# Performance work log

Measured on AMD Instinct MI355X. Metric: run time of the kernel, lower is better.

Reference implementation:

```python
import jax, jax.numpy as jnp
import numpy as np

CLAMP = 2.0
SPLIT1 = 48  # split_len1 (channels - channels//2)


def _down(x):
    # pixel-unshuffle: equivalent to the grouped stride-2 conv with 0/1 kernels
    B, C, H, W = x.shape
    x = x.reshape(B, C, H // 2, 2, W // 2, 2)
    x = x.transpose(0, 1, 3, 5, 2, 4)  # (B, C, di, dj, H/2, W/2)
    return x.reshape(B, C * 4, H // 2, W // 2)


def _conv(x, w, b, stride):
    y = jax.lax.conv_general_dilated(
        x, w, window_strides=(stride, stride), padding=[(1, 1), (1, 1)],
        dimension_numbers=('NCHW', 'OIHW', 'NCHW'))
    return y + b[None, :, None, None]


def _affine(x, a):
    # forward affine coupling: x * exp(clamp*tanh(0.2*a_s)) + a_t
    ch = x.shape[1]
    sub_jac = CLAMP * jnp.tanh(0.2 * a[:, :ch])
    return x * jnp.exp(sub_jac) + a[:, ch:]


def setup_inputs() -> dict:
    key = jax.random.key(0)
    ks = jax.random.split(key, 4)
    B, C, H, W = 32, 96, 64, 64
    s1, s2 = SPLIT1, C - SPLIT1
    x = jax.random.normal(ks[0], (B, C, H, W), jnp.float32)
    # s_hi: strided 3x3 conv, split_len1 -> 8*split_len2
    w_hi = jax.random.normal(ks[1], (8 * s2, s1, 3, 3), jnp.float32) * 0.05
    b_hi = jnp.zeros((8 * s2,), jnp.float32)
    # s_lo: same-res 3x3 conv, 4*split_len2 -> 8*split_len1
    w_lo = jax.random.normal(ks[2], (8 * s1, 4 * s2, 3, 3), jnp.float32) * 0.05
    b_lo = jnp.zeros((8 * s1,), jnp.float32)
    # actnorm params: act_norm init = 10.0 * 1.0 (SOFTPLUS branch)
    ch4 = 4 * C
    act_norm = jnp.full((1, ch4, 1, 1), 10.0, jnp.float32)
    act_offset = jnp.zeros((1, ch4, 1, 1), jnp.float32)
    # hard permutation matrix (permute_soft=False), fixed seed
    rng = np.random.default_rng(0)
    perm = rng.permutation(ch4)
    pw = np.zeros((ch4, ch4), np.float32)
    pw[np.arange(ch4), perm] = 1.0
    perm_w = jnp.asarray(pw)
    return dict(x=x, w_hi=w_hi, b_hi=b_hi, w_lo=w_lo, b_lo=b_lo,
                act_norm=act_norm, act_offset=act_offset, perm_w=perm_w)


def reference(x, w_hi, b_hi, w_lo, b_lo, act_norm, act_offset, perm_w):
    x1, x2 = x[:, :SPLIT1], x[:, SPLIT1:]
    y2 = _down(x2)                     # (B, 4*s2, H/2, W/2)
    a1 = _conv(x1, w_hi, b_hi, 2)      # (B, 8*s2, H/2, W/2)
    y2 = _affine(y2, a1)
    y1 = _down(x1)                     # (B, 4*s1, H/2, W/2)
    a2 = _conv(y2, w_lo, b_lo, 1)      # (B, 8*s1, H/2, W/2)
    y1 = _affine(y1, a2)
    out = jnp.concatenate([y1, y2], axis=1)  # (B, 4*C, H/2, W/2)
    # actnorm (SOFTPLUS: 0.1 * softplus_{beta=0.5}) + hard 1x1 permutation
    scale = 0.2 * jax.nn.softplus(0.5 * act_norm)
    out = jnp.einsum('bchw,oc->bohw', out * scale + act_offset, perm_w)
    return out
```

## Files before the change

kernel.cpp:

```cpp
#include <hip/hip_runtime.h>
#include <hip/hip_bf16.h>

typedef __attribute__((ext_vector_type(8))) short s16x8;
typedef __attribute__((ext_vector_type(4))) short s16x4;
typedef __attribute__((ext_vector_type(4))) float f32x4;
typedef unsigned short u16;

#define WS_FWD    0
#define WS_INV    2048
#define WS_SCALE  4096
#define WS_OFFS   6144
#define WS_WHI    8192
#define WS_WLO    14680064
#define WS_Y2     16777216

static __device__ __forceinline__ u16 f2bf(float f) {
    __hip_bfloat16 h = __float2bfloat16(f);
    return *reinterpret_cast<u16*>(&h);
}
static __device__ __forceinline__ float bf2f(u16 u) {
    __hip_bfloat16 h = *reinterpret_cast<__hip_bfloat16*>(&u);
    return __bfloat162float(h);
}

static __device__ __forceinline__ void gl_lds16(const void* g, void* l) {
    __builtin_amdgcn_global_load_lds(
        (const __attribute__((address_space(1))) unsigned int*)g,
        (__attribute__((address_space(3))) unsigned int*)l, 16, 0, 0);
}


__global__ __launch_bounds__(256)
void k_setup(const float* __restrict__ pw, const float* __restrict__ an,
             const float* __restrict__ ao, const float* __restrict__ w_hi,
             const float* __restrict__ w_lo, int* __restrict__ fwd,
             int* __restrict__ inv, float* __restrict__ scale,
             float* __restrict__ offs, u16* __restrict__ whi,
             u16* __restrict__ wlo)
{
    const int blk = blockIdx.x;
    const int tid = threadIdx.x;
    if (blk < 288) {
        int gid = blk * 256 + tid;
        int n = gid / 192;
        int c = gid - n * 192;
        int kc = c >> 5, c32 = c & 31;
        const float* src = w_lo + (size_t)gid * 9;
#pragma unroll
        for (int t = 0; t < 9; ++t)
            wlo[((size_t)(t * 6 + kc) * 384 + n) * 32 + c32] = f2bf(src[t]);
    } else if (blk < 576) {
        int gid = (blk - 288) * 256 + tid;
        int n = gid / 192;
        int c = gid - n * 192;
        int kc = c >> 5, c32 = c & 31;
        int cin = c >> 2, dy = (c >> 1) & 1, dx = c & 1;
        const float* src = w_hi + ((size_t)n * 48 + cin) * 9;
#pragma unroll
        for (int t = 0; t < 4; ++t) {
            int th = t >> 1, tw = t & 1;
            float wv = 0.f;
            if (!(th == 0 && dy == 0) && !(tw == 0 && dx == 0)) {
                int ky = (th == 0) ? 0 : 1 + dy;
                int kx = (tw == 0) ? 0 : 1 + dx;
                wv = src[ky * 3 + kx];
            }
            whi[((size_t)(t * 6 + kc) * 384 + n) * 32 + c32] = f2bf(wv);
        }
    } else {
        int gid = (blk - 576) * 256 + tid;
        int o = gid / 384;
        int c = gid - o * 384;
        if (pw[gid] > 0.5f) { fwd[o] = c; inv[c] = o; }
        if (gid < 384) {
            scale[gid] = 0.2f * log1pf(expf(0.5f * an[gid]));
            offs[gid]  = ao[gid];
        }
    }
}

template <int T>
__global__ __launch_bounds__(256)
void f_gemm(const u16* __restrict__ in_t, const u16* __restrict__ wpk,
            const float* __restrict__ bias, const float* __restrict__ x,
            const int* __restrict__ inv, const float* __restrict__ scale,
            const float* __restrict__ offs, u16* __restrict__ y2out,
            float* __restrict__ out)
{
    const int tid = threadIdx.x;
    const int lane = tid & 63;
    const int wave = tid >> 6;
    const int l16 = lane & 15;
    const int quad = lane >> 4;
    const int mblk = blockIdx.x;
    const int b = mblk >> 4;
    const int h0 = (mblk & 15) << 1;
    const int n0 = wave * 96;

    __shared__ u16 sm[384 * 68];

    const s16x8 zero8 = {0, 0, 0, 0, 0, 0, 0, 0};

    if (T == 4) {
        for (int r = 0; r < 4; ++r) {
            int ih = h0 - 1 + r;
            if (ih >= 0 && ih < 32) {
#pragma unroll
                for (int it = 0; it < 6; ++it) {
                    int k = it * 256 + tid;
                    int cin = k >> 5;
                    int dy = (k >> 4) & 1;
                    int q = k & 15;
                    f32x4 v = *(const f32x4*)&x[((size_t)(b * 96 + cin) * 64
                                                 + (2 * ih + dy)) * 64 + q * 4];
                    int ce = cin * 4 + dy * 2;
                    int g = ce >> 3;
                    int w0 = 2 * q, w1 = w0 + 1;
                    unsigned p0 = (unsigned)f2bf(v[0]) | ((unsigned)f2bf(v[1]) << 16);
                    unsigned p1 = (unsigned)f2bf(v[2]) | ((unsigned)f2bf(v[3]) << 16);
                    *(unsigned*)&sm[r * 6144 + w0 * 192 + ((g ^ (w0 & 7)) << 3) + (ce & 7)] = p0;
                    *(unsigned*)&sm[r * 6144 + w1 * 192 + ((g ^ (w1 & 7)) << 3) + (ce & 7)] = p1;
                }
            } else {
#pragma unroll
                for (int z = 0; z < 12; ++z)
                    ((unsigned*)&sm[r * 6144])[z * 256 + tid] = 0u;
            }
        }
    } else {
        for (int r = 0; r < 4; ++r) {
            int ih = h0 - 1 + r;
            if (ih >= 0 && ih < 32) {
                const char* gsrc = (const char*)in_t + ((size_t)b * 32 + ih) * 12288;
#pragma unroll
                for (int j = 0; j < 3; ++j) {
                    int off = j * 4096 + tid * 16;
                    gl_lds16(gsrc + off, (char*)sm + r * 12288 + off);
                }
            } else {
#pragma unroll
                for (int j = 0; j < 3; ++j)
                    *(s16x8*)((char*)sm + r * 12288 + j * 4096 + tid * 16) = zero8;
            }
        }
    }
    __syncthreads();

    const f32x4 zero4 = {0.f, 0.f, 0.f, 0.f};
    f32x4 acc[4][6];
#pragma unroll
    for (int a = 0; a < 4; ++a)
#pragma unroll
        for (int c = 0; c < 6; ++c) acc[a][c] = zero4;

    for (int t = 0; t < T; ++t) {
        const int dh = (T == 4) ? ((t >> 1) - 1) : (t / 3 - 1);
        const int dw = (T == 4) ? ((t & 1) - 1) : (t % 3 - 1);
#pragma unroll
        for (int kc = 0; kc < 6; ++kc) {
            const u16* wp = wpk + ((size_t)(t * 6 + kc) * 384) * 32;
            s16x8 bf[6];
#pragma unroll
            for (int ns = 0; ns < 6; ++ns)
                bf[ns] = *(const s16x8*)(wp + (n0 + ns * 16 + l16) * 32 + quad * 8);
            const int g = kc * 4 + quad;
            s16x8 af[4];
#pragma unroll
            for (int ms = 0; ms < 4; ++ms) {
                int m = ms * 16 + l16;
                int r = (m >> 5) + dh + 1;
                int iw = (m & 31) + dw;
                int iwc = iw < 0 ? 0 : (iw > 31 ? 31 : iw);
                s16x8 v = *(const s16x8*)&sm[r * 6144 + iwc * 192 + ((g ^ (iwc & 7)) << 3)];
                if (iw != iwc) v = zero8;
                af[ms] = v;
            }
#pragma unroll
            for (int ms = 0; ms < 4; ++ms)
#pragma unroll
                for (int ns = 0; ns < 6; ++ns)
                    acc[ms][ns] = __builtin_amdgcn_mfma_f32_16x16x32_bf16(
                        af[ms], bf[ns], acc[ms][ns], 0, 0, 0);
        }
    }

    __syncthreads();

#pragma unroll
    for (int ms = 0; ms < 4; ++ms) {
#pragma unroll
        for (int ns = 0; ns < 6; ++ns) {
            int n = n0 + ns * 16 + l16;
            float bv = bias[n];
            s16x4 pk;
#pragma unroll
            for (int r4 = 0; r4 < 4; ++r4)
                pk[r4] = (short)f2bf(acc[ms][ns][r4] + bv);
            *(s16x4*)&sm[n * 68 + ms * 16 + quad * 4] = pk;
        }
    }
    __syncthreads();

    {
        const int m = lane;
        const int h = h0 + (m >> 5);
        const int w = m & 31;
        for (int i = 0; i < 48; ++i) {
            int c = wave * 48 + i;
            float a_s = bf2f(sm[c * 68 + m]);
            float a_o = bf2f(sm[(c + 192) * 68 + m]);
            int cin = (T == 4 ? 48 : 0) + (c >> 2);
            float xv = x[(((size_t)b * 96 + cin) * 64 + (2 * h + ((c >> 1) & 1))) * 64
                         + (2 * w + (c & 1))];
            float e = expf(0.4f * a_s);
            float sj = 2.f - 4.f / (e + 1.f);
            float y = xv * expf(sj) + a_o;
            int cg = (T == 4) ? (192 + c) : c;
            int o = inv[cg];
            if (T == 4) {
                u16 yb = f2bf(y);
                sm[c * 68 + m] = yb;
                out[(((size_t)b * 384 + o) * 32 + h) * 32 + w] =
                    bf2f(yb) * scale[cg] + offs[cg];
            } else {
                out[(((size_t)b * 384 + o) * 32 + h) * 32 + w] =
                    y * scale[cg] + offs[cg];
            }
        }
    }

    if (T == 4) {
        __syncthreads();
        for (int it = 0; it < 6; ++it) {
            int v = it * 256 + tid;
            int m2 = v / 24;
            int c8 = v - m2 * 24;
            int c0 = c8 * 8;
            int h2 = h0 + (m2 >> 5);
            int w2 = m2 & 31;
            s16x8 yv;
#pragma unroll
            for (int j = 0; j < 8; ++j)
                yv[j] = (short)sm[(c0 + j) * 68 + m2];
            size_t off = ((size_t)b * 32 + h2) * 6144 + w2 * 192 + ((c8 ^ (w2 & 7)) << 3);
            *(s16x8*)&y2out[off] = yv;
        }
    }
}

extern "C" void kernel_launch(void* const* d_in, const int* in_sizes, int n_in,
                              void* d_out, int out_size, void* d_ws, size_t ws_size,
                              hipStream_t stream)
{
    const float* x        = (const float*)d_in[0];
    const float* w_hi     = (const float*)d_in[1];
    const float* b_hi     = (const float*)d_in[2];
    const float* w_lo     = (const float*)d_in[3];
    const float* b_lo     = (const float*)d_in[4];
    const float* act_norm = (const float*)d_in[5];
    const float* act_off  = (const float*)d_in[6];
    const float* perm_w   = (const float*)d_in[7];
    float* out = (float*)d_out;
    char* ws = (char*)d_ws;

    int*   fwd   = (int*)(ws + WS_FWD);
    int*   inv   = (int*)(ws + WS_INV);
    float* scale = (float*)(ws + WS_SCALE);
    float* offs  = (float*)(ws + WS_OFFS);
    u16*   whi   = (u16*)(ws + WS_WHI);
    u16*   wlo   = (u16*)(ws + WS_WLO);
    u16*   y2    = (u16*)(ws + WS_Y2);

    k_setup<<<1152, 256, 0, stream>>>(perm_w, act_norm, act_off, w_hi, w_lo,
                                      fwd, inv, scale, offs, whi, wlo);
    f_gemm<4><<<512, 256, 0, stream>>>(y2, whi, b_hi, x, inv, scale, offs, y2, out);
    f_gemm<9><<<512, 256, 0, stream>>>(y2, wlo, b_lo, x, inv, scale, offs, y2, out);
}
```

Baseline: 206.4 us.

## Pack weight conversion in pairs, swizzle block order, raise MFMA priority

The setup kernel now has each thread convert two adjacent input channels and write them as one 32-bit packed bf16 store, which halves the thread count and the number of narrow stores. The GEMM kernels remap blockIdx so that consecutive blocks are spread across batch/row groups, likely to balance work or cache locality across XCDs. MFMA sections are wrapped in s_setprio to favour the issuing wave. Each change is small, and the benefit depends on setup cost and scheduling effects.

```diff
diff --git a/kernel.cpp b/kernel.cpp
--- a/kernel.cpp
+++ b/kernel.cpp
@@ -40,35 +40,44 @@
 {
     const int blk = blockIdx.x;
     const int tid = threadIdx.x;
-    if (blk < 288) {
+    if (blk < 144) {
         int gid = blk * 256 + tid;
-        int n = gid / 192;
-        int c = gid - n * 192;
-        int kc = c >> 5, c32 = c & 31;
-        const float* src = w_lo + (size_t)gid * 9;
-#pragma unroll
-        for (int t = 0; t < 9; ++t)
-            wlo[((size_t)(t * 6 + kc) * 384 + n) * 32 + c32] = f2bf(src[t]);
-    } else if (blk < 576) {
-        int gid = (blk - 288) * 256 + tid;
-        int n = gid / 192;
-        int c = gid - n * 192;
-        int kc = c >> 5, c32 = c & 31;
-        int cin = c >> 2, dy = (c >> 1) & 1, dx = c & 1;
+        int n = gid / 96;
+        int cp = gid - n * 96;
+        int kc = cp >> 4, j = cp & 15;
+        int c = kc * 32 + 2 * j;
+        const float* src = w_lo + ((size_t)n * 192 + c) * 9;
+#pragma unroll
+        for (int t = 0; t < 9; ++t) {
+            unsigned pk = (unsigned)f2bf(src[t]) | ((unsigned)f2bf(src[9 + t]) << 16);
+            *(unsigned*)&wlo[((size_t)(t * 6 + kc) * 384 + n) * 32 + 2 * j] = pk;
+        }
+    } else if (blk < 288) {
+        int gid = (blk - 144) * 256 + tid;
+        int n = gid / 96;
+        int cp = gid - n * 96;
+        int kc = cp >> 4, j = cp & 15;
+        int c = kc * 32 + 2 * j;
+        int cin = c >> 2, dy = (c >> 1) & 1;
         const float* src = w_hi + ((size_t)n * 48 + cin) * 9;
 #pragma unroll
         for (int t = 0; t < 4; ++t) {
             int th = t >> 1, tw = t & 1;
-            float wv = 0.f;
-            if (!(th == 0 && dy == 0) && !(tw == 0 && dx == 0)) {
+            float wv0 = 0.f, wv1 = 0.f;
+            if (!(th == 0 && dy == 0)) {
                 int ky = (th == 0) ? 0 : 1 + dy;
-                int kx = (tw == 0) ? 0 : 1 + dx;
-                wv = src[ky * 3 + kx];
-            }
-            whi[((size_t)(t * 6 + kc) * 384 + n) * 32 + c32] = f2bf(wv);
+                if (tw != 0) {
+                    wv0 = src[ky * 3 + 1];
+                    wv1 = src[ky * 3 + 2];
+                } else {
+                    wv1 = src[ky * 3 + 0];
+                }
+            }
+            unsigned pk = (unsigned)f2bf(wv0) | ((unsigned)f2bf(wv1) << 16);
+            *(unsigned*)&whi[((size_t)(t * 6 + kc) * 384 + n) * 32 + 2 * j] = pk;
         }
     } else {
-        int gid = (blk - 576) * 256 + tid;
+        int gid = (blk - 288) * 256 + tid;
         int o = gid / 384;
         int c = gid - o * 384;
         if (pw[gid] > 0.5f) { fwd[o] = c; inv[c] = o; }
@@ -92,7 +101,7 @@
     const int wave = tid >> 6;
     const int l16 = lane & 15;
     const int quad = lane >> 4;
-    const int mblk = blockIdx.x;
+    const int mblk = ((blockIdx.x & 7) << 6) | (blockIdx.x >> 3);
     const int b = mblk >> 4;
     const int h0 = (mblk & 15) << 1;
     const int n0 = wave * 96;
@@ -175,12 +184,14 @@
                 if (iw != iwc) v = zero8;
                 af[ms] = v;
             }
+            __builtin_amdgcn_s_setprio(1);
 #pragma unroll
             for (int ms = 0; ms < 4; ++ms)
 #pragma unroll
                 for (int ns = 0; ns < 6; ++ns)
                     acc[ms][ns] = __builtin_amdgcn_mfma_f32_16x16x32_bf16(
                         af[ms], bf[ns], acc[ms][ns], 0, 0, 0);
+            __builtin_amdgcn_s_setprio(0);
         }
     }
 
@@ -271,8 +282,8 @@
     u16*   wlo   = (u16*)(ws + WS_WLO);
     u16*   y2    = (u16*)(ws + WS_Y2);
 
-    k_setup<<<1152, 256, 0, stream>>>(perm_w, act_norm, act_off, w_hi, w_lo,
-                                      fwd, inv, scale, offs, whi, wlo);
+    k_setup<<<864, 256, 0, stream>>>(perm_w, act_norm, act_off, w_hi, w_lo,
+                                     fwd, inv, scale, offs, whi, wlo);
     f_gemm<4><<<512, 256, 0, stream>>>(y2, whi, b_hi, x, inv, scale, offs, y2, out);
     f_gemm<9><<<512, 256, 0, stream>>>(y2, wlo, b_lo, x, inv, scale, offs, y2, out);
 }
```

Measured after the change: 218.5 us. 1.06x slower.
